# Optimization experiments

Hardware: AMD Instinct MI355X
Metric: run time of the kernel (lower is better)

## Reference

```python
import jax, jax.numpy as jnp
import numpy as np

B, C, H, W = 8, 64, 56, 56
PLANES = 64
EPS = 1e-5


def conv2d(x, w, b, stride=1, pad=1):
    out = jax.lax.conv_general_dilated(
        x, w, window_strides=(stride, stride), padding=[(pad, pad), (pad, pad)],
        dimension_numbers=('NCHW', 'OIHW', 'NCHW'))
    return out + b[None, :, None, None]


def _bilinear_gather(img, py, px):
    # img: [C,H,W]; py/px: [K2,Ho,Wo] float sample coords; zero outside bounds
    Ci, Hi, Wi = img.shape
    y0 = jnp.floor(py); x0 = jnp.floor(px)
    wy1 = py - y0; wx1 = px - x0
    wy0 = 1.0 - wy1; wx0 = 1.0 - wx1

    def g(yc, xc):
        valid = ((yc >= 0) & (yc < Hi) & (xc >= 0) & (xc < Wi)).astype(img.dtype)
        yi = jnp.clip(yc, 0, Hi - 1).astype(jnp.int32)
        xi = jnp.clip(xc, 0, Wi - 1).astype(jnp.int32)
        return img[:, yi, xi] * valid[None]  # [C,K2,Ho,Wo]

    return (g(y0, x0) * (wy0 * wx0)[None] + g(y0, x0 + 1) * (wy0 * wx1)[None]
            + g(y0 + 1, x0) * (wy1 * wx0)[None] + g(y0 + 1, x0 + 1) * (wy1 * wx1)[None])


def deform_conv2d(x, offset, weight, stride, pad, dil):
    # torchvision DeformConv2d semantics (no mask). offset: [B, 2*K2, Ho, Wo]
    Bx, Cx, Hx, Wx = x.shape
    O, _, kh, kw = weight.shape
    K2 = kh * kw
    Ho, Wo = offset.shape[2], offset.shape[3]
    off = offset.reshape(Bx, K2, 2, Ho, Wo)
    dy, dx = off[:, :, 0], off[:, :, 1]
    ki, kj = jnp.meshgrid(jnp.arange(kh), jnp.arange(kw), indexing='ij')
    base_y = (ki.reshape(-1) * dil - pad).astype(x.dtype)  # [K2]
    base_x = (kj.reshape(-1) * dil - pad).astype(x.dtype)
    hg = (jnp.arange(Ho) * stride).astype(x.dtype)
    wg = (jnp.arange(Wo) * stride).astype(x.dtype)
    py = dy + base_y[None, :, None, None] + hg[None, None, :, None]
    px = dx + base_x[None, :, None, None] + wg[None, None, None, :]
    cols = jax.vmap(_bilinear_gather)(x, py, px)  # [B,C,K2,Ho,Wo]
    return jnp.einsum('bckhw,ock->bohw', cols, weight.reshape(O, Cx, K2))


def bn(x, gamma, beta, mean, var):
    inv = gamma / jnp.sqrt(var + EPS)
    return x * inv[None, :, None, None] + (beta - mean * inv)[None, :, None, None]


def setup_inputs() -> dict:
    key = jax.random.key(0)
    ks = jax.random.split(key, 12)
    s = 0.05
    d = {
        'x':   jax.random.normal(ks[0], (B, C, H, W), jnp.float32),
        'ow1': jax.random.normal(ks[1], (2 * 9, C, 3, 3), jnp.float32) * s,
        'ob1': jnp.zeros((2 * 9,), jnp.float32),
        'ow3': jax.random.normal(ks[2], (2 * 25, C, 3, 3), jnp.float32) * s,
        'ob3': jnp.zeros((2 * 25,), jnp.float32),
        'ow2': jax.random.normal(ks[3], (2 * 9, PLANES, 3, 3), jnp.float32) * s,
        'ob2': jnp.zeros((2 * 9,), jnp.float32),
        'w1':  jax.random.normal(ks[4], (PLANES, C, 3, 3), jnp.float32) * s,
        'w3':  jax.random.normal(ks[5], (PLANES, C, 5, 5), jnp.float32) * s,
        'w2':  jax.random.normal(ks[6], (PLANES, PLANES, 3, 3), jnp.float32) * s,
    }
    for i, tag in zip((7, 8, 9), ('1', '3', '2')):
        d['g' + tag] = jnp.ones((PLANES,), jnp.float32)
        d['b' + tag] = jnp.zeros((PLANES,), jnp.float32)
        d['m' + tag] = jax.random.normal(ks[i], (PLANES,), jnp.float32) * 0.1
        d['v' + tag] = jnp.ones((PLANES,), jnp.float32)
    return d


def reference(x, ow1, ob1, ow3, ob3, ow2, ob2, w1, w3, w2,
              g1, b1, m1, v1, g3, b3, m3, v3, g2, b2, m2, v2):
    offset1 = conv2d(x, ow1, ob1, stride=1, pad=1)
    out = jax.nn.relu(bn(deform_conv2d(x, offset1, w1, 1, 2, 2), g1, b1, m1, v1))
    offset3 = conv2d(x, ow3, ob3, stride=1, pad=1)
    out_1 = jax.nn.relu(bn(deform_conv2d(x, offset3, w3, 1, 4, 2), g3, b3, m3, v3))
    out = out + out_1
    offset2 = conv2d(out, ow2, ob2, stride=1, pad=1)
    out = bn(deform_conv2d(out, offset2, w2, 1, 2, 2), g2, b2, m2, v2)
    out = out + x  # identity shortcut (stride=1, in_planes==planes)
    return jax.nn.relu(out)
```

## Files before the change

### kernel.cpp

```cpp
#include <hip/hip_runtime.h>
#include <math.h>

#define HD 56
#define WD 56
#define CD 64
#define PLANE 3136

typedef _Float16 f16x8 __attribute__((ext_vector_type(8)));
typedef _Float16 f16x4 __attribute__((ext_vector_type(4)));
typedef _Float16 f16x2 __attribute__((ext_vector_type(2)));
typedef float    f32x4 __attribute__((ext_vector_type(4)));

__global__ __launch_bounds__(256) void wtrans_k(
    const float* __restrict__ w1, const float* __restrict__ w3, const float* __restrict__ w2,
    const float* __restrict__ ow1, const float* __restrict__ ow3, const float* __restrict__ ow2,
    _Float16* __restrict__ t1, _Float16* __restrict__ t3, _Float16* __restrict__ t2,
    _Float16* __restrict__ owF, _Float16* __restrict__ owT2)
{
    int y = blockIdx.y;
    if (y == 0 || y == 1 || y == 2) {
        const float* src = (y == 0) ? w1 : (y == 1) ? w3 : w2;
        _Float16* dst    = (y == 0) ? t1 : (y == 1) ? t3 : t2;
        int K2 = (y == 1) ? 25 : 9;
        int total = 64 * 64 * K2;
        for (int idx = blockIdx.x * 256 + threadIdx.x; idx < total; idx += gridDim.x * 256) {
            int k = idx >> 12;
            int o = (idx >> 6) & 63;
            int c = idx & 63;
            dst[idx] = (_Float16)src[(o * 64 + c) * K2 + k];
        }
    } else if (y == 3) {
        int total = 9 * 32 * 64;
        for (int idx = blockIdx.x * 256 + threadIdx.x; idx < total; idx += gridDim.x * 256) {
            int k = idx >> 11;
            int o = (idx >> 6) & 31;
            int c = idx & 63;
            owF[k * 6144 + o * 64 + c] = (o < 18) ? (_Float16)ow1[(o * 64 + c) * 9 + k] : (_Float16)0.f;
        }
    } else if (y == 4) {
        int total = 9 * 64 * 64;
        for (int idx = blockIdx.x * 256 + threadIdx.x; idx < total; idx += gridDim.x * 256) {
            int k = idx >> 12;
            int o = (idx >> 6) & 63;
            int c = idx & 63;
            owF[k * 6144 + (32 + o) * 64 + c] = (o < 50) ? (_Float16)ow3[(o * 64 + c) * 9 + k] : (_Float16)0.f;
        }
    } else {
        int total = 9 * 32 * 64;
        for (int idx = blockIdx.x * 256 + threadIdx.x; idx < total; idx += gridDim.x * 256) {
            int k = idx >> 11;
            int o = (idx >> 6) & 31;
            int c = idx & 63;
            owT2[k * 2048 + o * 64 + c] = (o < 18) ? (_Float16)ow2[(o * 64 + c) * 9 + k] : (_Float16)0.f;
        }
    }
}

__global__ __launch_bounds__(256) void xt_k(const float* __restrict__ src, _Float16* __restrict__ dst)
{
    int b  = blockIdx.y;
    int px = blockIdx.x * 64 + (threadIdx.x & 63);
    int cg = threadIdx.x >> 6;
    const float* s = src + (size_t)b * CD * PLANE + px;
    f16x8 lo, hi;
#pragma unroll
    for (int i = 0; i < 8; ++i) lo[i] = (_Float16)s[(cg * 16 + i) * PLANE];
#pragma unroll
    for (int i = 0; i < 8; ++i) hi[i] = (_Float16)s[(cg * 16 + 8 + i) * PLANE];
    _Float16* d = dst + ((size_t)b * PLANE + px) * 64 + cg * 16;
    *(f16x8*)d = lo;
    *(f16x8*)(d + 8) = hi;
}

template<int FUSED>
__global__ __launch_bounds__(256) void offc_k(
    const _Float16* __restrict__ src,
    const _Float16* __restrict__ ow,
    const float* __restrict__ biasA, const float* __restrict__ biasB,
    uint4* __restrict__ tbl)
{
    constexpr int NTILES = FUSED ? 6 : 2;
    constexpr int OP     = FUSED ? 96 : 32;
    constexpr int NTT    = FUSED ? 34 : 9;
    __shared__ float red[4][NTILES * 4 * 64];

    int tid = threadIdx.x;
    int bid = blockIdx.x;
    int b    = bid & 7;
    int tile = bid >> 3;
    int l = tid & 63;
    int n = l & 15;
    int g = l >> 4;
    int w = tid >> 6;
    int kh = w & 1;
    int tg = w >> 1;
    int pix = tile * 16 + n;
    int ho = pix / WD, wo = pix - ho * WD;
    int ckoff = kh * 32 + g * 8;
    const _Float16* sp = src + ((size_t)b * PLANE + pix) * 64 + ckoff;

    f32x4 acc[NTILES];
#pragma unroll
    for (int t = 0; t < NTILES; ++t) acc[t] = (f32x4){0.f, 0.f, 0.f, 0.f};

#define OFFC_TAP(K)                                                            \
    {                                                                          \
        int ky = (K) / 3 - 1, kx = (K) % 3 - 1;                                \
        int yn = ho + ky, xn = wo + kx;                                        \
        f16x8 bf = {(_Float16)0, (_Float16)0, (_Float16)0, (_Float16)0,        \
                    (_Float16)0, (_Float16)0, (_Float16)0, (_Float16)0};       \
        if ((unsigned)yn < (unsigned)HD && (unsigned)xn < (unsigned)WD)        \
            bf = *(const f16x8*)(sp + (ky * WD + kx) * 64);                    \
        const _Float16* wk = ow + (K) * (OP * 64);                             \
        _Pragma("unroll")                                                      \
        for (int t = 0; t < NTILES; ++t) {                                     \
            f16x8 af = *(const f16x8*)(wk + (t * 16 + n) * 64 + ckoff);        \
            acc[t] = __builtin_amdgcn_mfma_f32_16x16x32_f16(af, bf, acc[t], 0, 0, 0); \
        }                                                                      \
    }

    if (tg == 0) {
#pragma unroll
        for (int k = 0; k < 5; ++k) OFFC_TAP(k)
    } else {
#pragma unroll
        for (int k = 5; k < 9; ++k) OFFC_TAP(k)
    }
#undef OFFC_TAP

#pragma unroll
    for (int t = 0; t < NTILES; ++t)
#pragma unroll
        for (int rr = 0; rr < 4; ++rr)
            red[w][(t * 4 + rr) * 64 + l] = acc[t][rr];
    __syncthreads();

#pragma unroll
    for (int tt = 0; tt < (NTILES + 3) / 4; ++tt) {
        int t = w + tt * 4;
        if (t < NTILES) {
            float v[4];
#pragma unroll
            for (int rr = 0; rr < 4; ++rr) {
                int ia = (t * 4 + rr) * 64 + l;
                v[rr] = red[0][ia] + red[1][ia] + red[2][ia] + red[3][ia];
            }
            int obase = t * 16 + g * 4;
            bool isB = FUSED && (t >= 2);
            int oc0 = isB ? (obase - 32) : obase;
            const float* bp = isB ? biasB : biasA;
#pragma unroll
            for (int pp = 0; pp < 2; ++pp) {
                int oce = oc0 + pp * 2;
                int kl  = oce >> 1;
                int kmax = isB ? 25 : 9;
                if (kl < kmax) {
                    float dy = v[pp * 2]     + bp[oce];
                    float dx = v[pp * 2 + 1] + bp[oce + 1];
                    int by, bx;
                    if (isB) { int q = kl / 5; by = q * 2 - 4; bx = (kl - q * 5) * 2 - 4; }
                    else     { int q = kl / 3; by = q * 2 - 2; bx = (kl - q * 3) * 2 - 2; }
                    float py = dy + (float)(by + ho);
                    float px = dx + (float)(bx + wo);
                    float fy = floorf(py), fx = floorf(px);
                    float wy1 = py - fy, wx1 = px - fx;
                    float wy0 = 1.f - wy1, wx0 = 1.f - wx1;
                    int y0 = (int)fy, x0 = (int)fx;
                    int y1 = y0 + 1, x1 = x0 + 1;
                    float vy0 = (y0 >= 0 && y0 < HD) ? 1.f : 0.f;
                    float vy1 = (y1 >= 0 && y1 < HD) ? 1.f : 0.f;
                    float vx0 = (x0 >= 0 && x0 < WD) ? 1.f : 0.f;
                    float vx1 = (x1 >= 0 && x1 < WD) ? 1.f : 0.f;
                    int cy0 = min(max(y0, 0), HD - 1), cy1 = min(max(y1, 0), HD - 1);
                    int cx0 = min(max(x0, 0), WD - 1), cx1 = min(max(x1, 0), WD - 1);
                    unsigned i00 = (unsigned)(cy0 * WD + cx0), i01 = (unsigned)(cy0 * WD + cx1);
                    unsigned i10 = (unsigned)(cy1 * WD + cx0), i11 = (unsigned)(cy1 * WD + cx1);
                    f16x2 wl = {(_Float16)(wy0 * wx0 * vy0 * vx0), (_Float16)(wy0 * wx1 * vy0 * vx1)};
                    f16x2 wh = {(_Float16)(wy1 * wx0 * vy1 * vx0), (_Float16)(wy1 * wx1 * vy1 * vx1)};
                    uint4 e;
                    e.x = i00 | (i01 << 16);
                    e.y = i10 | (i11 << 16);
                    e.z = __builtin_bit_cast(unsigned int, wl);
                    e.w = __builtin_bit_cast(unsigned int, wh);
                    int gtap = isB ? (9 + kl) : kl;
                    tbl[((size_t)(b * NTT + gtap)) * PLANE + pix] = e;
                }
            }
        }
    }
}

template<int MERGED>
__global__ __launch_bounds__(256) void dconv_k(
    const _Float16* __restrict__ xt,
    const uint4* __restrict__ tbl,
    const _Float16* __restrict__ wTA, const _Float16* __restrict__ wTB,
    const float* __restrict__ gA, const float* __restrict__ bA,
    const float* __restrict__ mA, const float* __restrict__ vA,
    const float* __restrict__ gB, const float* __restrict__ bB,
    const float* __restrict__ mB, const float* __restrict__ vB,
    const float* __restrict__ addsrc, float* __restrict__ out,
    _Float16* __restrict__ outh)
{
    constexpr int NT   = MERGED ? 34 : 9;
    constexpr int HALF = MERGED ? 17 : 5;
    constexpr int RS   = MERGED ? 32 : 16;
    __shared__ float red[3][RS * 64];

    int tid = threadIdx.x;
    int bid = blockIdx.x;
    int b    = bid & 7;
    int tile = bid >> 3;
    int l   = tid & 63;
    int n   = l & 15;
    int g   = l >> 4;
    int w   = tid >> 6;
    int kh  = w & 1;
    int tg  = w >> 1;
    int pix = tile * 16 + n;
    int ckoff = kh * 32 + g * 8;
    int base = tg ? HALF : 0;
    int cnt  = tg ? (NT - HALF) : HALF;

    const _Float16* xp = xt + (size_t)b * PLANE * 64 + ckoff;
    const uint4*    tp = tbl + (size_t)b * NT * PLANE + pix;
    int afoff = n * 64 + ckoff;

    f32x4 accA[4], accB[4];
#pragma unroll
    for (int ot = 0; ot < 4; ++ot) {
        accA[ot] = (f32x4){0.f, 0.f, 0.f, 0.f};
        accB[ot] = (f32x4){0.f, 0.f, 0.f, 0.f};
    }

    f16x8 v00, v01, v10, v11, af0, af1, af2, af3;
    _Float16 w0, w1, w2, w3;
    uint4 e_cur;

    {
        uint4 e0 = tp[base * PLANE];
        int t1 = (cnt > 1) ? base + 1 : base;
        e_cur = tp[t1 * PLANE];
        unsigned i00 = e0.x & 0xffffu, i01 = e0.x >> 16;
        unsigned i10 = e0.y & 0xffffu, i11 = e0.y >> 16;
        v00 = *(const f16x8*)(xp + i00 * 64);
        v01 = *(const f16x8*)(xp + i01 * 64);
        v10 = *(const f16x8*)(xp + i10 * 64);
        v11 = *(const f16x8*)(xp + i11 * 64);
        const _Float16* wk = (!MERGED || base < 9) ? (wTA + base * 4096) : (wTB + (base - 9) * 4096);
        af0 = *(const f16x8*)(wk + afoff);
        af1 = *(const f16x8*)(wk + afoff + 1024);
        af2 = *(const f16x8*)(wk + afoff + 2048);
        af3 = *(const f16x8*)(wk + afoff + 3072);
        f16x2 wl = __builtin_bit_cast(f16x2, e0.z);
        f16x2 wh = __builtin_bit_cast(f16x2, e0.w);
        w0 = wl.x; w1 = wl.y; w2 = wh.x; w3 = wh.y;
    }

#pragma unroll 2
    for (int j = 0; j < cnt; ++j) {
        int tap = base + j;
        bool hn = (j + 1 < cnt);
        f16x8 nv00, nv01, nv10, nv11, naf0, naf1, naf2, naf3;
        uint4 e_nxt;
        if (hn) {
            int t2 = (j + 2 < cnt) ? (tap + 2) : (base + cnt - 1);
            e_nxt = tp[t2 * PLANE];
            unsigned i00 = e_cur.x & 0xffffu, i01 = e_cur.x >> 16;
            unsigned i10 = e_cur.y & 0xffffu, i11 = e_cur.y >> 16;
            nv00 = *(const f16x8*)(xp + i00 * 64);
            nv01 = *(const f16x8*)(xp + i01 * 64);
            nv10 = *(const f16x8*)(xp + i10 * 64);
            nv11 = *(const f16x8*)(xp + i11 * 64);
            const _Float16* wk = (!MERGED || tap + 1 < 9) ? (wTA + (tap + 1) * 4096)
                                                          : (wTB + (tap - 8) * 4096);
            naf0 = *(const f16x8*)(wk + afoff);
            naf1 = *(const f16x8*)(wk + afoff + 1024);
            naf2 = *(const f16x8*)(wk + afoff + 2048);
            naf3 = *(const f16x8*)(wk + afoff + 3072);
        }
        f16x8 bf = v00 * w0 + v01 * w1 + v10 * w2 + v11 * w3;
        if (!MERGED || tap < 9) {
            accA[0] = __builtin_amdgcn_mfma_f32_16x16x32_f16(af0, bf, accA[0], 0, 0, 0);
            accA[1] = __builtin_amdgcn_mfma_f32_16x16x32_f16(af1, bf, accA[1], 0, 0, 0);
            accA[2] = __builtin_amdgcn_mfma_f32_16x16x32_f16(af2, bf, accA[2], 0, 0, 0);
            accA[3] = __builtin_amdgcn_mfma_f32_16x16x32_f16(af3, bf, accA[3], 0, 0, 0);
        } else {
            accB[0] = __builtin_amdgcn_mfma_f32_16x16x32_f16(af0, bf, accB[0], 0, 0, 0);
            accB[1] = __builtin_amdgcn_mfma_f32_16x16x32_f16(af1, bf, accB[1], 0, 0, 0);
            accB[2] = __builtin_amdgcn_mfma_f32_16x16x32_f16(af2, bf, accB[2], 0, 0, 0);
            accB[3] = __builtin_amdgcn_mfma_f32_16x16x32_f16(af3, bf, accB[3], 0, 0, 0);
        }
        if (hn) {
            v00 = nv00; v01 = nv01; v10 = nv10; v11 = nv11;
            af0 = naf0; af1 = naf1; af2 = naf2; af3 = naf3;
            f16x2 wl = __builtin_bit_cast(f16x2, e_cur.z);
            f16x2 wh = __builtin_bit_cast(f16x2, e_cur.w);
            w0 = wl.x; w1 = wl.y; w2 = wh.x; w3 = wh.y;
            e_cur = e_nxt;
        }
    }

    if (w > 0) {
#pragma unroll
        for (int ot = 0; ot < 4; ++ot)
#pragma unroll
            for (int rr = 0; rr < 4; ++rr) {
                red[w - 1][(ot * 4 + rr) * 64 + l] = accA[ot][rr];
                if (MERGED) red[w - 1][(16 + ot * 4 + rr) * 64 + l] = accB[ot][rr];
            }
    }
    __syncthreads();
    if (w == 0) {
#pragma unroll
        for (int ot = 0; ot < 4; ++ot) {
            float r[4];
#pragma unroll
            for (int rr = 0; rr < 4; ++rr) {
                int ia = (ot * 4 + rr) * 64 + l;
                float aA = accA[ot][rr] + red[0][ia] + red[1][ia] + red[2][ia];
                int o = ot * 16 + g * 4 + rr;
                float ivA = gA[o] * (1.f / sqrtf(vA[o] + 1e-5f));
                float shA = bA[o] - mA[o] * ivA;
                float vA_ = aA * ivA + shA;
                if (MERGED) {
                    int ib = (16 + ot * 4 + rr) * 64 + l;
                    float aB = accB[ot][rr] + red[0][ib] + red[1][ib] + red[2][ib];
                    float ivB = gB[o] * (1.f / sqrtf(vB[o] + 1e-5f));
                    float shB = bB[o] - mB[o] * ivB;
                    float vB_ = aB * ivB + shB;
                    r[rr] = fmaxf(vA_, 0.f) + fmaxf(vB_, 0.f);
                } else {
                    size_t oidx = (size_t)(b * 64 + o) * PLANE + pix;
                    out[oidx] = fmaxf(vA_ + addsrc[oidx], 0.f);
                }
            }
            if (MERGED) {
                f16x4 hv = {(_Float16)r[0], (_Float16)r[1], (_Float16)r[2], (_Float16)r[3]};
                *(f16x4*)(outh + ((size_t)b * PLANE + pix) * 64 + ot * 16 + g * 4) = hv;
            }
        }
    }
}

extern "C" void kernel_launch(void* const* d_in, const int* in_sizes, int n_in,
                              void* d_out, int out_size, void* d_ws, size_t ws_size,
                              hipStream_t stream) {
    const float* x   = (const float*)d_in[0];
    const float* ow1 = (const float*)d_in[1];
    const float* ob1 = (const float*)d_in[2];
    const float* ow3 = (const float*)d_in[3];
    const float* ob3 = (const float*)d_in[4];
    const float* ow2 = (const float*)d_in[5];
    const float* ob2 = (const float*)d_in[6];
    const float* w1  = (const float*)d_in[7];
    const float* w3  = (const float*)d_in[8];
    const float* w2  = (const float*)d_in[9];
    const float* g1  = (const float*)d_in[10];
    const float* b1  = (const float*)d_in[11];
    const float* m1  = (const float*)d_in[12];
    const float* v1  = (const float*)d_in[13];
    const float* g3  = (const float*)d_in[14];
    const float* b3  = (const float*)d_in[15];
    const float* m3  = (const float*)d_in[16];
    const float* v3  = (const float*)d_in[17];
    const float* g2  = (const float*)d_in[18];
    const float* b2  = (const float*)d_in[19];
    const float* m2  = (const float*)d_in[20];
    const float* v2  = (const float*)d_in[21];

    float* out = (float*)d_out;
    float* ws  = (float*)d_ws;

    _Float16* xth  = (_Float16*)ws;
    _Float16* mth  = (_Float16*)(ws + 802816);
    uint4*    tbl  = (uint4*)(ws + 1605632);
    _Float16* wT1h = (_Float16*)(ws + 5017600);
    _Float16* wT3h = wT1h + 36864;
    _Float16* wT2h = wT3h + 102400;
    _Float16* owFh = wT2h + 36864;
    _Float16* owT2h= owFh + 55296;

    wtrans_k<<<dim3(16, 6), dim3(256), 0, stream>>>(
        w1, w3, w2, ow1, ow3, ow2, wT1h, wT3h, wT2h, owFh, owT2h);
    xt_k<<<dim3(49, 8), dim3(256), 0, stream>>>(x, xth);

    offc_k<1><<<dim3(1568), dim3(256), 0, stream>>>(xth, owFh, ob1, ob3, tbl);

    dconv_k<1><<<dim3(1568), dim3(256), 0, stream>>>(
        xth, tbl, wT1h, wT3h, g1, b1, m1, v1, g3, b3, m3, v3, nullptr, nullptr, mth);

    offc_k<0><<<dim3(1568), dim3(256), 0, stream>>>(mth, owT2h, ob2, ob2, tbl);

    dconv_k<0><<<dim3(1568), dim3(256), 0, stream>>>(
        mth, tbl, wT2h, wT2h, g2, b2, m2, v2, g2, b2, m2, v2, x, out, nullptr);
}
```

Before: 200.7 us.

## Split merged deform conv across eight waves and double-buffer gather pipelines

The merged deformable-conv kernel now runs with 512 threads. Its eight waves each own a tap group (9/9/8/8 taps across the two K-halves), so every wave needs only one set of accumulators instead of separate A and B sets. The tap loop becomes an explicit two-stage ping-pong that issues the gathers and weight loads two taps ahead, with a shared-memory reduction sized for the extra waves. The offset-conv kernel also preloads all neighbour fragments and double-buffers its weight-fragment loads. In exchange, the larger blocks raise register pressure and shared-memory reduction traffic per block.

```diff
diff --git a/kernel.cpp b/kernel.cpp
--- a/kernel.cpp
+++ b/kernel.cpp
@@ -72,6 +72,13 @@
     *(f16x8*)(d + 8) = hi;
 }
 
+template<int NTILES, int OP>
+__device__ inline void af_load(const _Float16* __restrict__ ow, int k, int off, f16x8* s) {
+    const _Float16* wk = ow + k * (OP * 64);
+#pragma unroll
+    for (int t = 0; t < NTILES; ++t) s[t] = *(const f16x8*)(wk + (t * 16) * 64 + off);
+}
+
 template<int FUSED>
 __global__ __launch_bounds__(256) void offc_k(
     const _Float16* __restrict__ src,
@@ -92,41 +99,49 @@
     int n = l & 15;
     int g = l >> 4;
     int w = tid >> 6;
-    int kh = w & 1;
     int tg = w >> 1;
     int pix = tile * 16 + n;
     int ho = pix / WD, wo = pix - ho * WD;
-    int ckoff = kh * 32 + g * 8;
+    int ckoff = (w & 1) * 32 + g * 8;
+    int afo = n * 64 + ckoff;
     const _Float16* sp = src + ((size_t)b * PLANE + pix) * 64 + ckoff;
 
     f32x4 acc[NTILES];
 #pragma unroll
     for (int t = 0; t < NTILES; ++t) acc[t] = (f32x4){0.f, 0.f, 0.f, 0.f};
 
-#define OFFC_TAP(K)                                                            \
-    {                                                                          \
-        int ky = (K) / 3 - 1, kx = (K) % 3 - 1;                                \
-        int yn = ho + ky, xn = wo + kx;                                        \
-        f16x8 bf = {(_Float16)0, (_Float16)0, (_Float16)0, (_Float16)0,        \
-                    (_Float16)0, (_Float16)0, (_Float16)0, (_Float16)0};       \
-        if ((unsigned)yn < (unsigned)HD && (unsigned)xn < (unsigned)WD)        \
-            bf = *(const f16x8*)(sp + (ky * WD + kx) * 64);                    \
-        const _Float16* wk = ow + (K) * (OP * 64);                             \
-        _Pragma("unroll")                                                      \
-        for (int t = 0; t < NTILES; ++t) {                                     \
-            f16x8 af = *(const f16x8*)(wk + (t * 16 + n) * 64 + ckoff);        \
-            acc[t] = __builtin_amdgcn_mfma_f32_16x16x32_f16(af, bf, acc[t], 0, 0, 0); \
-        }                                                                      \
-    }
-
+#define NB(K, D) { int ky_=(K)/3-1, kx_=(K)%3-1; int yn_=ho+ky_, xn_=wo+kx_;       \
+    f16x8 z_ = {(_Float16)0,(_Float16)0,(_Float16)0,(_Float16)0,                   \
+                (_Float16)0,(_Float16)0,(_Float16)0,(_Float16)0};                  \
+    D = z_;                                                                        \
+    if ((unsigned)yn_ < (unsigned)HD && (unsigned)xn_ < (unsigned)WD)              \
+        D = *(const f16x8*)(sp + (ky_ * WD + kx_) * 64); }
+
+#define MFMAS(S, NBV) { _Pragma("unroll")                                          \
+    for (int t = 0; t < NTILES; ++t)                                               \
+        acc[t] = __builtin_amdgcn_mfma_f32_16x16x32_f16((S)[t], NBV, acc[t], 0, 0, 0); }
+
+    f16x8 sA[NTILES], sB[NTILES];
     if (tg == 0) {
-#pragma unroll
-        for (int k = 0; k < 5; ++k) OFFC_TAP(k)
+        f16x8 nb0, nb1, nb2, nb3, nb4;
+        NB(0, nb0) NB(1, nb1) NB(2, nb2) NB(3, nb3) NB(4, nb4)
+        af_load<NTILES, OP>(ow, 0, afo, sA);
+        af_load<NTILES, OP>(ow, 1, afo, sB); MFMAS(sA, nb0)
+        af_load<NTILES, OP>(ow, 2, afo, sA); MFMAS(sB, nb1)
+        af_load<NTILES, OP>(ow, 3, afo, sB); MFMAS(sA, nb2)
+        af_load<NTILES, OP>(ow, 4, afo, sA); MFMAS(sB, nb3)
+        MFMAS(sA, nb4)
     } else {
-#pragma unroll
-        for (int k = 5; k < 9; ++k) OFFC_TAP(k)
-    }
-#undef OFFC_TAP
+        f16x8 nb0, nb1, nb2, nb3;
+        NB(5, nb0) NB(6, nb1) NB(7, nb2) NB(8, nb3)
+        af_load<NTILES, OP>(ow, 5, afo, sA);
+        af_load<NTILES, OP>(ow, 6, afo, sB); MFMAS(sA, nb0)
+        af_load<NTILES, OP>(ow, 7, afo, sA); MFMAS(sB, nb1)
+        af_load<NTILES, OP>(ow, 8, afo, sB); MFMAS(sA, nb2)
+        MFMAS(sB, nb3)
+    }
+#undef NB
+#undef MFMAS
 
 #pragma unroll
     for (int t = 0; t < NTILES; ++t)
@@ -191,7 +206,7 @@
 }
 
 template<int MERGED>
-__global__ __launch_bounds__(256) void dconv_k(
+__global__ __launch_bounds__(MERGED ? 512 : 256) void dconv_k(
     const _Float16* __restrict__ xt,
     const uint4* __restrict__ tbl,
     const _Float16* __restrict__ wTA, const _Float16* __restrict__ wTB,
@@ -202,10 +217,9 @@
     const float* __restrict__ addsrc, float* __restrict__ out,
     _Float16* __restrict__ outh)
 {
-    constexpr int NT   = MERGED ? 34 : 9;
-    constexpr int HALF = MERGED ? 17 : 5;
-    constexpr int RS   = MERGED ? 32 : 16;
-    __shared__ float red[3][RS * 64];
+    constexpr int NT = MERGED ? 34 : 9;
+    constexpr int NW = MERGED ? 8 : 4;
+    __shared__ float red[NW - 1][16 * 64];
 
     int tid = threadIdx.x;
     int bid = blockIdx.x;
@@ -219,96 +233,83 @@
     int tg  = w >> 1;
     int pix = tile * 16 + n;
     int ckoff = kh * 32 + g * 8;
-    int base = tg ? HALF : 0;
-    int cnt  = tg ? (NT - HALF) : HALF;
+
+    int base, cnt;
+    if (MERGED) { base = (tg == 0) ? 0 : (tg == 1) ? 9 : (tg == 2) ? 18 : 26; cnt = (tg < 2) ? 9 : 8; }
+    else        { base = tg ? 5 : 0; cnt = tg ? 4 : 5; }
+    int lastT = base + cnt - 1;
 
     const _Float16* xp = xt + (size_t)b * PLANE * 64 + ckoff;
     const uint4*    tp = tbl + (size_t)b * NT * PLANE + pix;
     int afoff = n * 64 + ckoff;
 
-    f32x4 accA[4], accB[4];
-#pragma unroll
-    for (int ot = 0; ot < 4; ++ot) {
-        accA[ot] = (f32x4){0.f, 0.f, 0.f, 0.f};
-        accB[ot] = (f32x4){0.f, 0.f, 0.f, 0.f};
-    }
-
-    f16x8 v00, v01, v10, v11, af0, af1, af2, af3;
-    _Float16 w0, w1, w2, w3;
-    uint4 e_cur;
+    f32x4 acc[4];
+#pragma unroll
+    for (int ot = 0; ot < 4; ++ot) acc[ot] = (f32x4){0.f, 0.f, 0.f, 0.f};
+
+#define DECL_STG(S) f16x8 S##c0, S##c1, S##c2, S##c3, S##a0, S##a1, S##a2, S##a3; \
+                    unsigned S##wz, S##ww
+    DECL_STG(s0);
+    DECL_STG(s1);
+#undef DECL_STG
+
+#define ISSUE(S, E, T) {                                                      \
+    unsigned i00_ = (E).x & 0xffffu, i01_ = (E).x >> 16;                      \
+    unsigned i10_ = (E).y & 0xffffu, i11_ = (E).y >> 16;                      \
+    S##wz = (E).z; S##ww = (E).w;                                             \
+    S##c0 = *(const f16x8*)(xp + i00_ * 64);                                  \
+    S##c1 = *(const f16x8*)(xp + i01_ * 64);                                  \
+    S##c2 = *(const f16x8*)(xp + i10_ * 64);                                  \
+    S##c3 = *(const f16x8*)(xp + i11_ * 64);                                  \
+    const _Float16* wk_ = (!MERGED || (T) < 9) ? (wTA + (T) * 4096)           \
+                                               : (wTB + ((T) - 9) * 4096);    \
+    S##a0 = *(const f16x8*)(wk_ + afoff);                                     \
+    S##a1 = *(const f16x8*)(wk_ + afoff + 1024);                              \
+    S##a2 = *(const f16x8*)(wk_ + afoff + 2048);                              \
+    S##a3 = *(const f16x8*)(wk_ + afoff + 3072); }
+
+#define CONSUME(S) {                                                          \
+    f16x2 wl_ = __builtin_bit_cast(f16x2, S##wz);                             \
+    f16x2 wh_ = __builtin_bit_cast(f16x2, S##ww);                             \
+    f16x8 bf_ = S##c0 * wl_.x + S##c1 * wl_.y + S##c2 * wh_.x + S##c3 * wh_.y;\
+    acc[0] = __builtin_amdgcn_mfma_f32_16x16x32_f16(S##a0, bf_, acc[0], 0, 0, 0); \
+    acc[1] = __builtin_amdgcn_mfma_f32_16x16x32_f16(S##a1, bf_, acc[1], 0, 0, 0); \
+    acc[2] = __builtin_amdgcn_mfma_f32_16x16x32_f16(S##a2, bf_, acc[2], 0, 0, 0); \
+    acc[3] = __builtin_amdgcn_mfma_f32_16x16x32_f16(S##a3, bf_, acc[3], 0, 0, 0); }
 
     {
         uint4 e0 = tp[base * PLANE];
-        int t1 = (cnt > 1) ? base + 1 : base;
-        e_cur = tp[t1 * PLANE];
-        unsigned i00 = e0.x & 0xffffu, i01 = e0.x >> 16;
-        unsigned i10 = e0.y & 0xffffu, i11 = e0.y >> 16;
-        v00 = *(const f16x8*)(xp + i00 * 64);
-        v01 = *(const f16x8*)(xp + i01 * 64);
-        v10 = *(const f16x8*)(xp + i10 * 64);
-        v11 = *(const f16x8*)(xp + i11 * 64);
-        const _Float16* wk = (!MERGED || base < 9) ? (wTA + base * 4096) : (wTB + (base - 9) * 4096);
-        af0 = *(const f16x8*)(wk + afoff);
-        af1 = *(const f16x8*)(wk + afoff + 1024);
-        af2 = *(const f16x8*)(wk + afoff + 2048);
-        af3 = *(const f16x8*)(wk + afoff + 3072);
-        f16x2 wl = __builtin_bit_cast(f16x2, e0.z);
-        f16x2 wh = __builtin_bit_cast(f16x2, e0.w);
-        w0 = wl.x; w1 = wl.y; w2 = wh.x; w3 = wh.y;
-    }
-
-#pragma unroll 2
-    for (int j = 0; j < cnt; ++j) {
-        int tap = base + j;
-        bool hn = (j + 1 < cnt);
-        f16x8 nv00, nv01, nv10, nv11, naf0, naf1, naf2, naf3;
-        uint4 e_nxt;
-        if (hn) {
-            int t2 = (j + 2 < cnt) ? (tap + 2) : (base + cnt - 1);
-            e_nxt = tp[t2 * PLANE];
-            unsigned i00 = e_cur.x & 0xffffu, i01 = e_cur.x >> 16;
-            unsigned i10 = e_cur.y & 0xffffu, i11 = e_cur.y >> 16;
-            nv00 = *(const f16x8*)(xp + i00 * 64);
-            nv01 = *(const f16x8*)(xp + i01 * 64);
-            nv10 = *(const f16x8*)(xp + i10 * 64);
-            nv11 = *(const f16x8*)(xp + i11 * 64);
-            const _Float16* wk = (!MERGED || tap + 1 < 9) ? (wTA + (tap + 1) * 4096)
-                                                          : (wTB + (tap - 8) * 4096);
-            naf0 = *(const f16x8*)(wk + afoff);
-            naf1 = *(const f16x8*)(wk + afoff + 1024);
-            naf2 = *(const f16x8*)(wk + afoff + 2048);
-            naf3 = *(const f16x8*)(wk + afoff + 3072);
-        }
-        f16x8 bf = v00 * w0 + v01 * w1 + v10 * w2 + v11 * w3;
-        if (!MERGED || tap < 9) {
-            accA[0] = __builtin_amdgcn_mfma_f32_16x16x32_f16(af0, bf, accA[0], 0, 0, 0);
-            accA[1] = __builtin_amdgcn_mfma_f32_16x16x32_f16(af1, bf, accA[1], 0, 0, 0);
-            accA[2] = __builtin_amdgcn_mfma_f32_16x16x32_f16(af2, bf, accA[2], 0, 0, 0);
-            accA[3] = __builtin_amdgcn_mfma_f32_16x16x32_f16(af3, bf, accA[3], 0, 0, 0);
-        } else {
-            accB[0] = __builtin_amdgcn_mfma_f32_16x16x32_f16(af0, bf, accB[0], 0, 0, 0);
-            accB[1] = __builtin_amdgcn_mfma_f32_16x16x32_f16(af1, bf, accB[1], 0, 0, 0);
-            accB[2] = __builtin_amdgcn_mfma_f32_16x16x32_f16(af2, bf, accB[2], 0, 0, 0);
-            accB[3] = __builtin_amdgcn_mfma_f32_16x16x32_f16(af3, bf, accB[3], 0, 0, 0);
-        }
-        if (hn) {
-            v00 = nv00; v01 = nv01; v10 = nv10; v11 = nv11;
-            af0 = naf0; af1 = naf1; af2 = naf2; af3 = naf3;
-            f16x2 wl = __builtin_bit_cast(f16x2, e_cur.z);
-            f16x2 wh = __builtin_bit_cast(f16x2, e_cur.w);
-            w0 = wl.x; w1 = wl.y; w2 = wh.x; w3 = wh.y;
-            e_cur = e_nxt;
-        }
-    }
+        uint4 e1 = tp[(base + 1) * PLANE];
+        ISSUE(s0, e0, base)
+        ISSUE(s1, e1, base + 1)
+    }
+    uint4 E0 = tp[min(base + 2, lastT) * PLANE];
+    uint4 E1 = tp[min(base + 3, lastT) * PLANE];
+
+    int j = 0;
+#pragma unroll 1
+    for (; j + 1 < cnt; j += 2) {
+        CONSUME(s0)
+        if (j + 2 < cnt) {
+            ISSUE(s0, E0, base + j + 2)
+            E0 = tp[min(base + j + 4, lastT) * PLANE];
+        }
+        CONSUME(s1)
+        if (j + 3 < cnt) {
+            ISSUE(s1, E1, base + j + 3)
+            E1 = tp[min(base + j + 5, lastT) * PLANE];
+        }
+    }
+    if (j < cnt) CONSUME(s0)
+#undef ISSUE
+#undef CONSUME
 
     if (w > 0) {
 #pragma unroll
         for (int ot = 0; ot < 4; ++ot)
 #pragma unroll
-            for (int rr = 0; rr < 4; ++rr) {
-                red[w - 1][(ot * 4 + rr) * 64 + l] = accA[ot][rr];
-                if (MERGED) red[w - 1][(16 + ot * 4 + rr) * 64 + l] = accB[ot][rr];
-            }
+            for (int rr = 0; rr < 4; ++rr)
+                red[w - 1][(ot * 4 + rr) * 64 + l] = acc[ot][rr];
     }
     __syncthreads();
     if (w == 0) {
@@ -318,21 +319,22 @@
 #pragma unroll
             for (int rr = 0; rr < 4; ++rr) {
                 int ia = (ot * 4 + rr) * 64 + l;
-                float aA = accA[ot][rr] + red[0][ia] + red[1][ia] + red[2][ia];
                 int o = ot * 16 + g * 4 + rr;
-                float ivA = gA[o] * (1.f / sqrtf(vA[o] + 1e-5f));
-                float shA = bA[o] - mA[o] * ivA;
-                float vA_ = aA * ivA + shA;
                 if (MERGED) {
-                    int ib = (16 + ot * 4 + rr) * 64 + l;
-                    float aB = accB[ot][rr] + red[0][ib] + red[1][ib] + red[2][ib];
+                    float sumA = acc[ot][rr] + red[0][ia];
+                    float sumB = red[1][ia] + red[2][ia] + red[3][ia]
+                               + red[4][ia] + red[5][ia] + red[6][ia];
+                    float ivA = gA[o] * (1.f / sqrtf(vA[o] + 1e-5f));
+                    float shA = bA[o] - mA[o] * ivA;
                     float ivB = gB[o] * (1.f / sqrtf(vB[o] + 1e-5f));
                     float shB = bB[o] - mB[o] * ivB;
-                    float vB_ = aB * ivB + shB;
-                    r[rr] = fmaxf(vA_, 0.f) + fmaxf(vB_, 0.f);
+                    r[rr] = fmaxf(sumA * ivA + shA, 0.f) + fmaxf(sumB * ivB + shB, 0.f);
                 } else {
+                    float s = acc[ot][rr] + red[0][ia] + red[1][ia] + red[2][ia];
+                    float iv = gA[o] * (1.f / sqrtf(vA[o] + 1e-5f));
+                    float sh = bA[o] - mA[o] * iv;
                     size_t oidx = (size_t)(b * 64 + o) * PLANE + pix;
-                    out[oidx] = fmaxf(vA_ + addsrc[oidx], 0.f);
+                    out[oidx] = fmaxf(s * iv + sh + addsrc[oidx], 0.f);
                 }
             }
             if (MERGED) {
@@ -387,7 +389,7 @@
 
     offc_k<1><<<dim3(1568), dim3(256), 0, stream>>>(xth, owFh, ob1, ob3, tbl);
 
-    dconv_k<1><<<dim3(1568), dim3(256), 0, stream>>>(
+    dconv_k<1><<<dim3(1568), dim3(512), 0, stream>>>(
         xth, tbl, wT1h, wT3h, g1, b1, m1, v1, g3, b3, m3, v3, nullptr, nullptr, mth);
 
     offc_k<0><<<dim3(1568), dim3(256), 0, stream>>>(mth, owT2h, ob2, ob2, tbl);
```

New measurement: 201.7 us. About the same (+0.5%).

## Software-pipeline offset conv weight loads and pack two pixel tiles per dconv block

Applied to the files above, without the earlier changes.

In the offset conv kernel, all neighbour pixel vectors are loaded up front and the per-tap weight fragments are double-buffered, so each tap's loads overlap the previous tap's MFMAs. The deform conv kernel now runs 512 threads per block covering two 16-pixel tiles, which halves the grid and doubles the shared reduction buffer. The merged variant also splits its 34 taps evenly into 17 and 17. More registers are in flight in offc and shared memory per dconv block grows, which could lower occupancy.

```diff
diff --git a/kernel.cpp b/kernel.cpp
--- a/kernel.cpp
+++ b/kernel.cpp
@@ -72,6 +72,13 @@
     *(f16x8*)(d + 8) = hi;
 }
 
+template<int NTILES, int OP>
+__device__ inline void af_load(const _Float16* __restrict__ ow, int k, int off, f16x8* s) {
+    const _Float16* wk = ow + k * (OP * 64);
+#pragma unroll
+    for (int t = 0; t < NTILES; ++t) s[t] = *(const f16x8*)(wk + (t * 16) * 64 + off);
+}
+
 template<int FUSED>
 __global__ __launch_bounds__(256) void offc_k(
     const _Float16* __restrict__ src,
@@ -92,41 +99,49 @@
     int n = l & 15;
     int g = l >> 4;
     int w = tid >> 6;
-    int kh = w & 1;
     int tg = w >> 1;
     int pix = tile * 16 + n;
     int ho = pix / WD, wo = pix - ho * WD;
-    int ckoff = kh * 32 + g * 8;
+    int ckoff = (w & 1) * 32 + g * 8;
+    int afo = n * 64 + ckoff;
     const _Float16* sp = src + ((size_t)b * PLANE + pix) * 64 + ckoff;
 
     f32x4 acc[NTILES];
 #pragma unroll
     for (int t = 0; t < NTILES; ++t) acc[t] = (f32x4){0.f, 0.f, 0.f, 0.f};
 
-#define OFFC_TAP(K)                                                            \
-    {                                                                          \
-        int ky = (K) / 3 - 1, kx = (K) % 3 - 1;                                \
-        int yn = ho + ky, xn = wo + kx;                                        \
-        f16x8 bf = {(_Float16)0, (_Float16)0, (_Float16)0, (_Float16)0,        \
-                    (_Float16)0, (_Float16)0, (_Float16)0, (_Float16)0};       \
-        if ((unsigned)yn < (unsigned)HD && (unsigned)xn < (unsigned)WD)        \
-            bf = *(const f16x8*)(sp + (ky * WD + kx) * 64);                    \
-        const _Float16* wk = ow + (K) * (OP * 64);                             \
-        _Pragma("unroll")                                                      \
-        for (int t = 0; t < NTILES; ++t) {                                     \
-            f16x8 af = *(const f16x8*)(wk + (t * 16 + n) * 64 + ckoff);        \
-            acc[t] = __builtin_amdgcn_mfma_f32_16x16x32_f16(af, bf, acc[t], 0, 0, 0); \
-        }                                                                      \
-    }
-
+#define NB(K, D) { int ky_=(K)/3-1, kx_=(K)%3-1; int yn_=ho+ky_, xn_=wo+kx_;       \
+    f16x8 z_ = {(_Float16)0,(_Float16)0,(_Float16)0,(_Float16)0,                   \
+                (_Float16)0,(_Float16)0,(_Float16)0,(_Float16)0};                  \
+    D = z_;                                                                        \
+    if ((unsigned)yn_ < (unsigned)HD && (unsigned)xn_ < (unsigned)WD)              \
+        D = *(const f16x8*)(sp + (ky_ * WD + kx_) * 64); }
+
+#define MFMAS(S, NBV) { _Pragma("unroll")                                          \
+    for (int t = 0; t < NTILES; ++t)                                               \
+        acc[t] = __builtin_amdgcn_mfma_f32_16x16x32_f16((S)[t], NBV, acc[t], 0, 0, 0); }
+
+    f16x8 sA[NTILES], sB[NTILES];
     if (tg == 0) {
-#pragma unroll
-        for (int k = 0; k < 5; ++k) OFFC_TAP(k)
+        f16x8 nb0, nb1, nb2, nb3, nb4;
+        NB(0, nb0) NB(1, nb1) NB(2, nb2) NB(3, nb3) NB(4, nb4)
+        af_load<NTILES, OP>(ow, 0, afo, sA);
+        af_load<NTILES, OP>(ow, 1, afo, sB); MFMAS(sA, nb0)
+        af_load<NTILES, OP>(ow, 2, afo, sA); MFMAS(sB, nb1)
+        af_load<NTILES, OP>(ow, 3, afo, sB); MFMAS(sA, nb2)
+        af_load<NTILES, OP>(ow, 4, afo, sA); MFMAS(sB, nb3)
+        MFMAS(sA, nb4)
     } else {
-#pragma unroll
-        for (int k = 5; k < 9; ++k) OFFC_TAP(k)
-    }
-#undef OFFC_TAP
+        f16x8 nb0, nb1, nb2, nb3;
+        NB(5, nb0) NB(6, nb1) NB(7, nb2) NB(8, nb3)
+        af_load<NTILES, OP>(ow, 5, afo, sA);
+        af_load<NTILES, OP>(ow, 6, afo, sB); MFMAS(sA, nb0)
+        af_load<NTILES, OP>(ow, 7, afo, sA); MFMAS(sB, nb1)
+        af_load<NTILES, OP>(ow, 8, afo, sB); MFMAS(sA, nb2)
+        MFMAS(sB, nb3)
+    }
+#undef NB
+#undef MFMAS
 
 #pragma unroll
     for (int t = 0; t < NTILES; ++t)
@@ -191,7 +206,7 @@
 }
 
 template<int MERGED>
-__global__ __launch_bounds__(256) void dconv_k(
+__global__ __launch_bounds__(512) void dconv_k(
     const _Float16* __restrict__ xt,
     const uint4* __restrict__ tbl,
     const _Float16* __restrict__ wTA, const _Float16* __restrict__ wTB,
@@ -202,25 +217,28 @@
     const float* __restrict__ addsrc, float* __restrict__ out,
     _Float16* __restrict__ outh)
 {
-    constexpr int NT   = MERGED ? 34 : 9;
-    constexpr int HALF = MERGED ? 17 : 5;
-    constexpr int RS   = MERGED ? 32 : 16;
-    __shared__ float red[3][RS * 64];
+    constexpr int NT = MERGED ? 34 : 9;
+    constexpr int RS = MERGED ? 32 : 16;
+    __shared__ float red[2][3][RS * 64];
 
     int tid = threadIdx.x;
     int bid = blockIdx.x;
     int b    = bid & 7;
-    int tile = bid >> 3;
+    int tp2  = bid >> 3;
     int l   = tid & 63;
     int n   = l & 15;
     int g   = l >> 4;
     int w   = tid >> 6;
-    int kh  = w & 1;
-    int tg  = w >> 1;
+    int pr  = w & 1;
+    int kh  = (w >> 1) & 1;
+    int tg  = w >> 2;
+    int tile = tp2 * 2 + pr;
     int pix = tile * 16 + n;
     int ckoff = kh * 32 + g * 8;
-    int base = tg ? HALF : 0;
-    int cnt  = tg ? (NT - HALF) : HALF;
+
+    int base, cnt;
+    if (MERGED) { base = tg * 17; cnt = 17; }
+    else        { base = tg ? 5 : 0; cnt = tg ? 4 : 5; }
 
     const _Float16* xp = xt + (size_t)b * PLANE * 64 + ckoff;
     const uint4*    tp = tbl + (size_t)b * NT * PLANE + pix;
@@ -301,38 +319,40 @@
         }
     }
 
-    if (w > 0) {
+    int pidx = (tg << 1) | kh;
+    if (pidx > 0) {
 #pragma unroll
         for (int ot = 0; ot < 4; ++ot)
 #pragma unroll
             for (int rr = 0; rr < 4; ++rr) {
-                red[w - 1][(ot * 4 + rr) * 64 + l] = accA[ot][rr];
-                if (MERGED) red[w - 1][(16 + ot * 4 + rr) * 64 + l] = accB[ot][rr];
+                red[pr][pidx - 1][(ot * 4 + rr) * 64 + l] = accA[ot][rr];
+                if (MERGED) red[pr][pidx - 1][(16 + ot * 4 + rr) * 64 + l] = accB[ot][rr];
             }
     }
     __syncthreads();
-    if (w == 0) {
+    if (pidx == 0) {
 #pragma unroll
         for (int ot = 0; ot < 4; ++ot) {
             float r[4];
 #pragma unroll
             for (int rr = 0; rr < 4; ++rr) {
                 int ia = (ot * 4 + rr) * 64 + l;
-                float aA = accA[ot][rr] + red[0][ia] + red[1][ia] + red[2][ia];
                 int o = ot * 16 + g * 4 + rr;
-                float ivA = gA[o] * (1.f / sqrtf(vA[o] + 1e-5f));
-                float shA = bA[o] - mA[o] * ivA;
-                float vA_ = aA * ivA + shA;
                 if (MERGED) {
                     int ib = (16 + ot * 4 + rr) * 64 + l;
-                    float aB = accB[ot][rr] + red[0][ib] + red[1][ib] + red[2][ib];
+                    float sumA = accA[ot][rr] + red[pr][0][ia] + red[pr][1][ia] + red[pr][2][ia];
+                    float sumB = accB[ot][rr] + red[pr][0][ib] + red[pr][1][ib] + red[pr][2][ib];
+                    float ivA = gA[o] * (1.f / sqrtf(vA[o] + 1e-5f));
+                    float shA = bA[o] - mA[o] * ivA;
                     float ivB = gB[o] * (1.f / sqrtf(vB[o] + 1e-5f));
                     float shB = bB[o] - mB[o] * ivB;
-                    float vB_ = aB * ivB + shB;
-                    r[rr] = fmaxf(vA_, 0.f) + fmaxf(vB_, 0.f);
+                    r[rr] = fmaxf(sumA * ivA + shA, 0.f) + fmaxf(sumB * ivB + shB, 0.f);
                 } else {
+                    float s = accA[ot][rr] + red[pr][0][ia] + red[pr][1][ia] + red[pr][2][ia];
+                    float iv = gA[o] * (1.f / sqrtf(vA[o] + 1e-5f));
+                    float sh = bA[o] - mA[o] * iv;
                     size_t oidx = (size_t)(b * 64 + o) * PLANE + pix;
-                    out[oidx] = fmaxf(vA_ + addsrc[oidx], 0.f);
+                    out[oidx] = fmaxf(s * iv + sh + addsrc[oidx], 0.f);
                 }
             }
             if (MERGED) {
@@ -387,11 +407,11 @@
 
     offc_k<1><<<dim3(1568), dim3(256), 0, stream>>>(xth, owFh, ob1, ob3, tbl);
 
-    dconv_k<1><<<dim3(1568), dim3(256), 0, stream>>>(
+    dconv_k<1><<<dim3(784), dim3(512), 0, stream>>>(
         xth, tbl, wT1h, wT3h, g1, b1, m1, v1, g3, b3, m3, v3, nullptr, nullptr, mth);
 
     offc_k<0><<<dim3(1568), dim3(256), 0, stream>>>(mth, owT2h, ob2, ob2, tbl);
 
-    dconv_k<0><<<dim3(1568), dim3(256), 0, stream>>>(
+    dconv_k<0><<<dim3(784), dim3(512), 0, stream>>>(
         mth, tbl, wT2h, wT2h, g2, b2, m2, v2, g2, b2, m2, v2, x, out, nullptr);
 }
```

Result: slower. 219.3 us (+9.3%).
